# Performance work log

Measured on AMD Instinct MI355X. Metric: run time of the kernel, lower is better.

The kernel has to match this reference:

```python
import jax, jax.numpy as jnp
import numpy as np
from jax import lax

# Static config (matches init_kwargs / electrode montage)
B, T, V = 16, 1536, 64
F1, D, H = 16, 2, 4
F2 = F1 * D              # 32
FO = F2 // H             # 8, GAT per-head out dim
K1, K3 = 32, 16          # conv kernel sizes (temporal)
P1, P2 = 8, 4            # avg pool sizes
KNN = 4
EPS = 1e-5
NEG_SLOPE = 0.2          # PyG GATConv leaky_relu slope


def _build_edges():
    # deterministic electrode geometry -> kNN graph, plus PyG self-loops
    rng = np.random.RandomState(0)
    pos = rng.randn(V, 3)
    dmat = np.linalg.norm(pos[:, None] - pos[None, :], axis=-1)
    order = np.argsort(dmat, axis=1)
    nbrs = order[:, 1:KNN + 1]                      # exclude self
    src = np.repeat(np.arange(V), KNN)
    dst = nbrs.reshape(-1)
    # add self loops (GATConv default add_self_loops=True)
    src = np.concatenate([src, np.arange(V)])
    dst = np.concatenate([dst, np.arange(V)])
    return jnp.asarray(np.stack([src, dst]), dtype=jnp.int32)  # (2, E)


def _bn(x, g, b, m, v, axis):
    shp = [1] * x.ndim
    shp[axis] = -1
    rs = lambda a: a.reshape(shp)
    return rs(g) * (x - rs(m)) * lax.rsqrt(rs(v) + EPS) + rs(b)


def _conv_same_t(x, w, k):
    # Conv2d(..., (1,k), padding='same'): torch pads (k-1)//2 left, rest right
    lp = (k - 1) // 2
    return lax.conv_general_dilated(x, w, (1, 1), [(0, 0), (lp, k - 1 - lp)],
                                    dimension_numbers=('NCHW', 'OIHW', 'NCHW'))


def _gat(x, W, a_src, a_dst, bias, src, dst):
    # Batched PyG GATConv (eval mode, dropout off), concat heads.
    # x: (Ng, V, F1); W: (F1, H*FO); a_src/a_dst: (H, FO); bias: (H*FO,)
    Ng = x.shape[0]
    h = jnp.einsum('nvf,fho->nvho', x, W.reshape(F1, H, FO))   # (Ng,V,H,FO)
    es = jnp.einsum('nvho,ho->nvh', h, a_src)[:, src]          # (Ng,E,H)
    ed = jnp.einsum('nvho,ho->nvh', h, a_dst)[:, dst]
    e = jax.nn.leaky_relu(es + ed, NEG_SLOPE)
    # softmax over incoming edges of each target node (segment softmax)
    m = jnp.full((Ng, V, H), -1e30, e.dtype).at[:, dst].max(e)
    ex = jnp.exp(e - m[:, dst])
    den = jnp.zeros((Ng, V, H), e.dtype).at[:, dst].add(ex)
    alpha = ex / den[:, dst]                                   # (Ng,E,H)
    out = jnp.zeros((Ng, V, H, FO), e.dtype).at[:, dst].add(alpha[..., None] * h[:, src])
    return out.reshape(Ng, V, H * FO) + bias


def setup_inputs() -> dict:
    key = jax.random.key(0)
    ks = jax.random.split(key, 16)
    bn = lambda k, c: (1.0 + 0.1 * jax.random.normal(jax.random.fold_in(k, 0), (c,)),
                       0.1 * jax.random.normal(jax.random.fold_in(k, 1), (c,)),
                       0.1 * jax.random.normal(jax.random.fold_in(k, 2), (c,)),
                       0.5 + jax.random.uniform(jax.random.fold_in(k, 3), (c,)))
    bn1 = bn(ks[1], F1); bn2 = bn(ks[2], F2); bn3 = bn(ks[3], F2)
    inp = {
        'x': jax.random.normal(ks[0], (B, 1, V, T), jnp.float32),
        'conv1_w': 0.1 * jax.random.normal(ks[4], (F1, 1, 1, K1), jnp.float32),
        'bn1_g': bn1[0], 'bn1_b': bn1[1], 'bn1_m': bn1[2], 'bn1_v': bn1[3],
        'gat_w': (1.0 / np.sqrt(F1)) * jax.random.normal(ks[5], (F1, H * FO), jnp.float32),
        'gat_asrc': 0.3 * jax.random.normal(ks[6], (H, FO), jnp.float32),
        'gat_adst': 0.3 * jax.random.normal(ks[7], (H, FO), jnp.float32),
        'gat_bias': 0.05 * jax.random.normal(ks[8], (H * FO,), jnp.float32),
        'bn2_g': bn2[0], 'bn2_b': bn2[1], 'bn2_m': bn2[2], 'bn2_v': bn2[3],
        'conv3_w': 0.1 * jax.random.normal(ks[9], (F2, F2, 1, K3), jnp.float32),
        'bn3_g': bn3[0], 'bn3_b': bn3[1], 'bn3_m': bn3[2], 'bn3_v': bn3[3],
        'edge_index': _build_edges(),
    }
    return inp


def reference(x, conv1_w, bn1_g, bn1_b, bn1_m, bn1_v,
              gat_w, gat_asrc, gat_adst, gat_bias,
              bn2_g, bn2_b, bn2_m, bn2_v,
              conv3_w, bn3_g, bn3_b, bn3_m, bn3_v, edge_index):
    src, dst = edge_index[0], edge_index[1]
    # block1: temporal conv + BN
    h = _conv_same_t(x, conv1_w, K1)                 # (B,F1,V,T)
    h = _bn(h, bn1_g, bn1_b, bn1_m, bn1_v, 1)
    # spatial GNN over B*T independent electrode graphs
    xg = h.transpose(0, 3, 2, 1).reshape(B * T, V, F1)
    g = _gat(xg, gat_w, gat_asrc, gat_adst, gat_bias, src, dst)   # (BT,V,F2)
    g = g.mean(axis=1).reshape(B, T, F2).transpose(0, 2, 1)       # (B,F2,T)
    g = _bn(g, bn2_g, bn2_b, bn2_m, bn2_v, 1)[:, :, None, :]      # (B,F2,1,T)
    # tail: elu -> pool -> conv -> bn -> elu -> pool (dropout = eval no-op)
    h = jax.nn.elu(g)
    h = h.reshape(B, F2, 1, T // P1, P1).mean(-1)
    h = _conv_same_t(h, conv3_w, K3)
    h = _bn(h, bn3_g, bn3_b, bn3_m, bn3_v, 1)
    h = jax.nn.elu(h)
    h = h.reshape(B, F2, 1, T // P1 // P2, P2).mean(-1)           # (B,F2,1,48)
    return h
```

## Files before the change

kernel.cpp:

```cpp
#include <hip/hip_runtime.h>
#include <math.h>

#define TPB 256

constexpr int Bc = 16, Tc = 1536;
constexpr int T2c = 192;
constexpr float EPSc = 1e-5f;
constexpr float NSLOPE = 0.2f;
constexpr int MDI = 16;
constexpr int MDO = 8;

constexpr int OW_WEFF = 0;
constexpr int OW_CHL  = 1024;
constexpr int OW_CES  = 1056;
constexpr int OW_WES  = 1064;
constexpr int OW_WED  = 1192;
constexpr int OW_GRAPH= 1320;
constexpr int OW_P    = 1740;

constexpr int GB_INTS = 417;

constexpr int L_XT  = 0;
constexpr int L_WB  = 2720;
constexpr int L_Y   = 4896;
constexpr int L_WF  = 6208;
constexpr int L_CHL = 7232;
constexpr int L_GR  = 7264;
constexpr int L_TOT = 7681;
constexpr int L_G   = L_GR;

__global__ void prep_kernel(const float* __restrict__ c1w,
                            const float* __restrict__ g1, const float* __restrict__ b1,
                            const float* __restrict__ m1, const float* __restrict__ v1,
                            const float* __restrict__ W,
                            const float* __restrict__ asrc, const float* __restrict__ adst,
                            const int* __restrict__ ei, int ne, float* __restrict__ ws)
{
    const int tid = threadIdx.x;
    __shared__ float sweff[1024];
    __shared__ float schl[32];
    __shared__ int isrcp_i[64 * MDI];
    __shared__ int outdst_i[64 * MDO];
    __shared__ int inslot[64], outslot[64];

    for (int idx = tid; idx < 1024; idx += TPB) {
        int k = idx >> 5, f2 = idx & 31;
        float s = 0.f;
        for (int f = 0; f < 16; f++) {
            float a1 = g1[f] * rsqrtf(v1[f] + EPSc);
            s += a1 * W[f * 32 + f2] * c1w[f * 32 + k];
        }
        ws[OW_WEFF + idx] = s;
        sweff[idx] = s;
    }
    for (int f2 = tid; f2 < 32; f2 += TPB) {
        float s = 0.f;
        for (int f = 0; f < 16; f++) {
            float a1 = g1[f] * rsqrtf(v1[f] + EPSc);
            s = fmaf(b1[f] - a1 * m1[f], W[f * 32 + f2], s);
        }
        ws[OW_CHL + f2] = s;
        schl[f2] = s;
    }

    for (int i = tid; i < 64 * MDI; i += TPB) isrcp_i[i] = 0;
    for (int i = tid; i < 64 * MDO; i += TPB) outdst_i[i] = 0;
    if (tid < 64) { inslot[tid] = 0; outslot[tid] = 0; }
    __syncthreads();
    for (int e = tid; e < ne; e += TPB) {
        int s = ei[e], d = ei[ne + e];
        int pi = atomicAdd(&inslot[d], 1);
        if (pi < MDI) isrcp_i[d * MDI + pi] = s;
        int po = atomicAdd(&outslot[s], 1);
        if (po < MDO) outdst_i[s * MDO + po] = d;
    }
    __syncthreads();

    if (tid < 128) {
        int k = tid >> 2, h = tid & 3;
        float s1 = 0.f, s2 = 0.f;
        for (int o = 0; o < 8; o++) {
            float wv = sweff[k * 32 + h * 8 + o];
            s1 = fmaf(asrc[h * 8 + o], wv, s1);
            s2 = fmaf(adst[h * 8 + o], wv, s2);
        }
        ws[OW_WES + h * 32 + k] = s1;
        ws[OW_WED + h * 32 + k] = s2;
    }
    if (tid < 4) {
        float s1 = 0.f, s2 = 0.f;
        for (int o = 0; o < 8; o++) {
            float cv = schl[tid * 8 + o];
            s1 = fmaf(asrc[tid * 8 + o], cv, s1);
            s2 = fmaf(adst[tid * 8 + o], cv, s2);
        }
        ws[OW_CES + tid] = s1;
        ws[OW_CES + 4 + tid] = s2;
    }
    unsigned char* gb = (unsigned char*)(ws + OW_GRAPH);
    for (int i = tid; i < 64 * MDI; i += TPB) gb[i] = (unsigned char)isrcp_i[i];
    for (int i = tid; i < 64 * MDO; i += TPB) gb[1088 + i] = (unsigned char)outdst_i[i];
    if (tid < 64) {
        gb[1024 + tid] = (unsigned char)(inslot[tid] < MDI ? inslot[tid] : MDI);
        gb[1600 + tid] = (unsigned char)(outslot[tid] < MDO ? outslot[tid] : MDO);
    }
    __syncthreads();
    if (tid == 0) {
        int mi = 0, mo = 0;
        for (int d = 0; d < 64; d++) {
            int a = gb[1024 + d], o = gb[1600 + d];
            mi = a > mi ? a : mi;
            mo = o > mo ? o : mo;
        }
        gb[1664] = (unsigned char)mi;
        gb[1665] = (unsigned char)mo;
    }
}

__global__ __launch_bounds__(TPB, 5) void gat_kernel(
    const float* __restrict__ x,
    const float* __restrict__ wfp,
    const float* __restrict__ chlp,
    const float* __restrict__ cesg,
    const float* __restrict__ wesg,
    const float* __restrict__ wedg,
    const float* __restrict__ bias,
    const float* __restrict__ g2, const float* __restrict__ b2,
    const float* __restrict__ m2, const float* __restrict__ v2,
    const int* __restrict__ graphi,
    float* __restrict__ pout)
{
    __shared__ __align__(16) float sm[L_TOT];
    unsigned char* gb = (unsigned char*)&sm[L_GR];

    const int tid  = threadIdx.x;
    const int b    = blockIdx.x / 192;
    const int tile = blockIdx.x % 192;
    const int t0   = tile * 8;

    for (int idx = tid; idx < GB_INTS; idx += TPB) ((int*)&sm[L_GR])[idx] = graphi[idx];
    {
        const float4 w4 = ((const float4*)wfp)[tid];
        *(float4*)&sm[L_WF + tid * 4] = w4;
    }
    if (tid < 32) sm[L_CHL + tid] = chlp[tid];
    for (int idx = tid; idx < 2560; idx += TPB) {
        const int v = idx & 63, j = idx >> 6;
        float val = 1.0f;
        if (j < 39) {
            const int t = t0 - 15 + j;
            val = (t >= 0 && t < Tc) ? x[(b * 64 + v) * Tc + t] : 0.f;
        }
        sm[L_XT + j * 68 + v] = val;
    }
    __syncthreads();

    const int h = tid >> 6, v = tid & 63;
    const int hs = __builtin_amdgcn_readfirstlane(h);
    const float* wesh = wesg + hs * 32;
    const float* wedh = wedg + hs * 32;

    float aes[8], aed[8];
    {
        const float cesh = cesg[hs], cedh = cesg[4 + hs];
        #pragma unroll
        for (int t = 0; t < 8; t++) { aes[t] = cesh; aed[t] = cedh; }
        float xr[8];
        #pragma unroll
        for (int q = 0; q < 7; q++) xr[q] = sm[L_XT + q * 68 + v];
        #pragma unroll
        for (int k = 0; k < 32; k++) {
            xr[(k + 7) & 7] = sm[L_XT + (k + 7) * 68 + v];
            const float wek = wesh[k];
            const float wdk = wedh[k];
            #pragma unroll
            for (int t = 0; t < 8; t++) {
                const float xv = xr[(k + t) & 7];
                aes[t] = fmaf(xv, wek, aes[t]);
                aed[t] = fmaf(xv, wdk, aed[t]);
            }
        }
    }

    {
        const int indeg = gb[1024 + v];
        const int mdin  = gb[1664];
        float den[8] = { 0.f,0.f,0.f,0.f,0.f,0.f,0.f,0.f };
        for (int e = 0; e < mdin; e++) {
            const int s = gb[v * MDI + e];
            const float valid = (e < indeg) ? 1.f : 0.f;
            #pragma unroll
            for (int t = 0; t < 8; t++) {
                float ev = __shfl(aes[t], s) + aed[t];
                ev = ev > 0.f ? ev : NSLOPE * ev;
                den[t] += valid * __expf(ev);
            }
        }
        float rden[8];
        #pragma unroll
        for (int t = 0; t < 8; t++) rden[t] = 1.f / den[t];

        const int odeg = gb[1600 + v];
        const int mdo  = gb[1665];
        float wb[8] = { 0.f,0.f,0.f,0.f,0.f,0.f,0.f,0.f };
        for (int j = 0; j < mdo; j++) {
            const int d = gb[1088 + v * MDO + j];
            const float valid = (j < odeg) ? 1.f : 0.f;
            #pragma unroll
            for (int t = 0; t < 8; t++) {
                float ev = aes[t] + __shfl(aed[t], d);
                ev = ev > 0.f ? ev : NSLOPE * ev;
                wb[t] += valid * __expf(ev) * __shfl(rden[t], d);
            }
        }
        #pragma unroll
        for (int t = 0; t < 8; t++) sm[L_WB + h * 544 + t * 68 + v] = wb[t];
    }
    __asm__ volatile("s_waitcnt lgkmcnt(0)" ::: "memory");

    {
        const int t = v >> 3, cg = v & 7;
        float ya[5] = { 0.f, 0.f, 0.f, 0.f, 0.f };
        const float* wbbase = &sm[L_WB + h * 544 + t * 68];
        const float* xbase  = &sm[L_XT + cg * 5 * 68];
        for (int v4 = 0; v4 < 16; v4++) {
            const float4 w4 = *(const float4*)(wbbase + v4 * 4);
            #pragma unroll
            for (int q = 0; q < 5; q++) {
                const float4 x4 = *(const float4*)(xbase + q * 68 + v4 * 4);
                ya[q] = fmaf(w4.x, x4.x, fmaf(w4.y, x4.y,
                        fmaf(w4.z, x4.z, fmaf(w4.w, x4.w, ya[q]))));
            }
        }
        float* yr = &sm[L_Y + h * 328 + t * 41 + cg * 5];
        #pragma unroll
        for (int q = 0; q < 5; q++) yr[q] = ya[q];
    }
    __syncthreads();

    {
        const int t = v >> 3, o = v & 7, f2 = h * 8 + o;
        const float* yr = &sm[L_Y + h * 328 + t * 41];
        float acc = sm[L_CHL + f2] * yr[39];
        #pragma unroll
        for (int k = 0; k < 32; k++)
            acc = fmaf(sm[L_WF + k * 32 + f2], yr[t + k], acc);
        sm[L_G + t * 32 + f2] = acc;
    }
    __syncthreads();

    if (tid < 32) {
        const float a2 = g2[tid] * rsqrtf(v2[tid] + EPSc);
        const float c2 = b2[tid] + a2 * (bias[tid] - m2[tid]);
        float s = 0.f;
        #pragma unroll
        for (int t = 0; t < 8; t++) {
            const float gv = sm[L_G + t * 32 + tid] * (1.f / 64.f);
            const float y = fmaf(a2, gv, c2);
            s += y > 0.f ? y : __expf(y) - 1.f;
        }
        pout[(b * T2c + tile) * 32 + tid] = s * 0.125f;
    }
}

__global__ __launch_bounds__(TPB) void conv3_kernel(const float* __restrict__ pp,
                                                    const float* __restrict__ w3,
                                                    const float* __restrict__ g3,
                                                    const float* __restrict__ b3,
                                                    const float* __restrict__ m3,
                                                    const float* __restrict__ v3,
                                                    float* __restrict__ outp)
{
    __shared__ float w3s[16 * 1057];
    __shared__ float pl[63 * 32];
    __shared__ float q[48 * 32];
    const int tid = threadIdx.x;
    const int b = blockIdx.x >> 2, cc = blockIdx.x & 3;

    for (int idx4 = tid; idx4 < 4096; idx4 += TPB) {
        const float4 w4 = *(const float4*)(w3 + idx4 * 4);
        const int k0 = (idx4 * 4) & 15, f2i = (idx4 >> 2) & 31, f2o = idx4 >> 7;
        const float wq[4] = { w4.x, w4.y, w4.z, w4.w };
        #pragma unroll
        for (int j = 0; j < 4; j++)
            w3s[(k0 + j) * 1057 + f2i * 33 + f2o] = wq[j];
    }
    for (int idx = tid; idx < 63 * 32; idx += TPB) {
        int r = idx >> 5, f2 = idx & 31;
        int tog = cc * 48 - 7 + r;
        pl[idx] = (tog >= 0 && tog < T2c) ? pp[(b * T2c + tog) * 32 + f2] : 0.f;
    }
    __syncthreads();

    const int f2o = tid & 31, grp = tid >> 5;
    const int tb = grp * 6;
    float acc[6] = { 0.f, 0.f, 0.f, 0.f, 0.f, 0.f };
    for (int f2i = 0; f2i < 32; f2i++) {
        float seg[21];
        #pragma unroll
        for (int r = 0; r < 21; r++) seg[r] = pl[(tb + r) * 32 + f2i];
        #pragma unroll
        for (int k = 0; k < 16; k++) {
            float wv = w3s[k * 1057 + f2i * 33 + f2o];
            #pragma unroll
            for (int j = 0; j < 6; j++)
                acc[j] = fmaf(seg[j + k], wv, acc[j]);
        }
    }
    const float a3 = g3[f2o] * rsqrtf(v3[f2o] + EPSc);
    const float c3 = b3[f2o] - a3 * m3[f2o];
    #pragma unroll
    for (int j = 0; j < 6; j++) {
        float y = fmaf(a3, acc[j], c3);
        y = y > 0.f ? y : __expf(y) - 1.f;
        q[(tb + j) * 32 + f2o] = y;
    }
    __syncthreads();
    for (int idx = tid; idx < 12 * 32; idx += TPB) {
        int t4 = idx >> 5, f2 = idx & 31;
        int r0 = t4 * 4;
        float s = q[r0 * 32 + f2] + q[(r0 + 1) * 32 + f2] +
                  q[(r0 + 2) * 32 + f2] + q[(r0 + 3) * 32 + f2];
        outp[(b * 32 + f2) * 48 + cc * 12 + t4] = s * 0.25f;
    }
}

extern "C" void kernel_launch(void* const* d_in, const int* in_sizes, int n_in,
                              void* d_out, int out_size, void* d_ws, size_t ws_size,
                              hipStream_t stream)
{
    const float* x    = (const float*)d_in[0];
    const float* c1w  = (const float*)d_in[1];
    const float* g1   = (const float*)d_in[2];
    const float* b1   = (const float*)d_in[3];
    const float* m1   = (const float*)d_in[4];
    const float* v1   = (const float*)d_in[5];
    const float* W    = (const float*)d_in[6];
    const float* asrc = (const float*)d_in[7];
    const float* adst = (const float*)d_in[8];
    const float* bias = (const float*)d_in[9];
    const float* g2   = (const float*)d_in[10];
    const float* b2   = (const float*)d_in[11];
    const float* m2   = (const float*)d_in[12];
    const float* v2   = (const float*)d_in[13];
    const float* w3   = (const float*)d_in[14];
    const float* g3   = (const float*)d_in[15];
    const float* b3   = (const float*)d_in[16];
    const float* m3   = (const float*)d_in[17];
    const float* v3   = (const float*)d_in[18];
    const int*   ei   = (const int*)d_in[19];
    const int    ne   = in_sizes[19] / 2;

    float* ws = (float*)d_ws;

    prep_kernel<<<1, TPB, 0, stream>>>(c1w, g1, b1, m1, v1, W, asrc, adst,
                                       ei, ne, ws);

    gat_kernel<<<Bc * T2c, TPB, 0, stream>>>(x,
                                             ws + OW_WEFF, ws + OW_CHL,
                                             ws + OW_CES,
                                             ws + OW_WES, ws + OW_WED,
                                             bias, g2, b2, m2, v2,
                                             (const int*)(ws + OW_GRAPH),
                                             ws + OW_P);

    conv3_kernel<<<Bc * 4, TPB, 0, stream>>>(ws + OW_P, w3, g3, b3, m3, v3,
                                             (float*)d_out);
}
```

Before: 171.5 us.

## Keep GAT final weights in registers and read conv3 weights from global

In the GAT kernel, the final-projection weights and channel constants now sit in per-thread registers instead of shared memory. This shrinks the LDS footprint and raises the launch-bounds occupancy target from 5 to 6 blocks. In the conv3 kernel, the large transposed weight staging in shared memory is removed and each thread reads its weights directly from global memory as float4. The cost is more register pressure in the GAT kernel and uncached-pattern global loads in conv3. Note the float4 FMA chain sums each group of four taps in reverse order, which changes floating-point rounding slightly.

```diff
diff --git a/kernel.cpp b/kernel.cpp
--- a/kernel.cpp
+++ b/kernel.cpp
@@ -23,10 +23,8 @@
 constexpr int L_XT  = 0;
 constexpr int L_WB  = 2720;
 constexpr int L_Y   = 4896;
-constexpr int L_WF  = 6208;
-constexpr int L_CHL = 7232;
-constexpr int L_GR  = 7264;
-constexpr int L_TOT = 7681;
+constexpr int L_GR  = 6208;
+constexpr int L_TOT = 6625;
 constexpr int L_G   = L_GR;
 
 __global__ void prep_kernel(const float* __restrict__ c1w,
@@ -117,7 +115,7 @@
     }
 }
 
-__global__ __launch_bounds__(TPB, 5) void gat_kernel(
+__global__ __launch_bounds__(TPB, 6) void gat_kernel(
     const float* __restrict__ x,
     const float* __restrict__ wfp,
     const float* __restrict__ chlp,
@@ -138,24 +136,26 @@
     const int tile = blockIdx.x % 192;
     const int t0   = tile * 8;
 
+    const int h = tid >> 6, v = tid & 63;
+    const int f2d = h * 8 + (v & 7);
+
+    float wfr[32];
+    #pragma unroll
+    for (int k = 0; k < 32; k++) wfr[k] = wfp[k * 32 + f2d];
+    const float chld = chlp[f2d];
+
     for (int idx = tid; idx < GB_INTS; idx += TPB) ((int*)&sm[L_GR])[idx] = graphi[idx];
-    {
-        const float4 w4 = ((const float4*)wfp)[tid];
-        *(float4*)&sm[L_WF + tid * 4] = w4;
-    }
-    if (tid < 32) sm[L_CHL + tid] = chlp[tid];
     for (int idx = tid; idx < 2560; idx += TPB) {
-        const int v = idx & 63, j = idx >> 6;
+        const int vv = idx & 63, j = idx >> 6;
         float val = 1.0f;
         if (j < 39) {
             const int t = t0 - 15 + j;
-            val = (t >= 0 && t < Tc) ? x[(b * 64 + v) * Tc + t] : 0.f;
-        }
-        sm[L_XT + j * 68 + v] = val;
-    }
-    __syncthreads();
-
-    const int h = tid >> 6, v = tid & 63;
+            val = (t >= 0 && t < Tc) ? x[(b * 64 + vv) * Tc + t] : 0.f;
+        }
+        sm[L_XT + j * 68 + vv] = val;
+    }
+    __syncthreads();
+
     const int hs = __builtin_amdgcn_readfirstlane(h);
     const float* wesh = wesg + hs * 32;
     const float* wedh = wedg + hs * 32;
@@ -239,13 +239,13 @@
     __syncthreads();
 
     {
-        const int t = v >> 3, o = v & 7, f2 = h * 8 + o;
+        const int t = v >> 3;
         const float* yr = &sm[L_Y + h * 328 + t * 41];
-        float acc = sm[L_CHL + f2] * yr[39];
+        float acc = chld * yr[39];
         #pragma unroll
         for (int k = 0; k < 32; k++)
-            acc = fmaf(sm[L_WF + k * 32 + f2], yr[t + k], acc);
-        sm[L_G + t * 32 + f2] = acc;
+            acc = fmaf(wfr[k], yr[t + k], acc);
+        sm[L_G + t * 32 + f2d] = acc;
     }
     __syncthreads();
 
@@ -271,20 +271,11 @@
                                                     const float* __restrict__ v3,
                                                     float* __restrict__ outp)
 {
-    __shared__ float w3s[16 * 1057];
     __shared__ float pl[63 * 32];
     __shared__ float q[48 * 32];
     const int tid = threadIdx.x;
     const int b = blockIdx.x >> 2, cc = blockIdx.x & 3;
 
-    for (int idx4 = tid; idx4 < 4096; idx4 += TPB) {
-        const float4 w4 = *(const float4*)(w3 + idx4 * 4);
-        const int k0 = (idx4 * 4) & 15, f2i = (idx4 >> 2) & 31, f2o = idx4 >> 7;
-        const float wq[4] = { w4.x, w4.y, w4.z, w4.w };
-        #pragma unroll
-        for (int j = 0; j < 4; j++)
-            w3s[(k0 + j) * 1057 + f2i * 33 + f2o] = wq[j];
-    }
     for (int idx = tid; idx < 63 * 32; idx += TPB) {
         int r = idx >> 5, f2 = idx & 31;
         int tog = cc * 48 - 7 + r;
@@ -299,12 +290,17 @@
         float seg[21];
         #pragma unroll
         for (int r = 0; r < 21; r++) seg[r] = pl[(tb + r) * 32 + f2i];
-        #pragma unroll
-        for (int k = 0; k < 16; k++) {
-            float wv = w3s[k * 1057 + f2i * 33 + f2o];
-            #pragma unroll
-            for (int j = 0; j < 6; j++)
-                acc[j] = fmaf(seg[j + k], wv, acc[j]);
+        const float4* wrow = (const float4*)(w3 + (f2o * 32 + f2i) * 16);
+        #pragma unroll
+        for (int k4 = 0; k4 < 4; k4++) {
+            const float4 w4 = wrow[k4];
+            #pragma unroll
+            for (int j = 0; j < 6; j++) {
+                acc[j] = fmaf(seg[j + k4 * 4 + 0], w4.x,
+                         fmaf(seg[j + k4 * 4 + 1], w4.y,
+                         fmaf(seg[j + k4 * 4 + 2], w4.z,
+                         fmaf(seg[j + k4 * 4 + 3], w4.w, acc[j]))));
+            }
         }
     }
     const float a3 = g3[f2o] * rsqrtf(v3[f2o] + EPSc);
```

New measurement: 176.4 us. 2.8% more time.
